# Optimization experiments

Hardware: AMD Instinct MI355X
Metric: run time of the kernel (lower is better)

Reference implementation:

```python
import jax, jax.numpy as jnp
import numpy as np

YOLO_INTERVAL = 20.0
N_BOXES = 4_000_000
N_ANCHORS = 5
N_CELLS = 12  # image_size // yolo_interval


def setup_inputs() -> dict:
    key = jax.random.key(0)
    k1, k2, k3 = jax.random.split(key, 3)
    cell_nos = jax.random.randint(k1, (N_BOXES, 2), 0, N_CELLS, dtype=jnp.int32)
    output = jax.random.uniform(k2, (N_BOXES, N_ANCHORS, 5), dtype=jnp.float32)
    target = jax.random.uniform(k3, (N_BOXES, 5), dtype=jnp.float32)
    return {"cell_nos": cell_nos, "output": output, "target": target}


def _bbox_to_corners(cell_nos, dx, dy, h, w):
    # cell_nos: [N,2] int; dx,dy,h,w: [N,K] float. Returns [N,K,4] (x1,y1,x2,y2).
    yi = YOLO_INTERVAL
    h = h * yi
    w = w * yi
    cell_i_center = cell_nos[:, 0:1].astype(dx.dtype) * yi + yi / 2  # [N,1]
    cell_j_center = cell_nos[:, 1:2].astype(dx.dtype) * yi + yi / 2
    x_center = cell_i_center + dx * yi  # broadcast [N,K]
    y_center = cell_j_center + dy * yi
    x1 = y_center - w / 2
    y1 = x_center - h / 2
    x2 = y_center + w / 2
    y2 = x_center + h / 2
    return jnp.stack([x1, y1, x2, y2], axis=-1)


def reference(cell_nos, output, target):
    # Predicted boxes: [N, A, 4]
    dxp, dyp, hp, wp = (output[:, :, i] for i in range(1, 5))
    bbox_pred = _bbox_to_corners(cell_nos, dxp, dyp, hp, wp)
    # Ground-truth boxes: [N, 4]
    dxg, dyg, hg, wg = (target[:, i:i + 1] for i in range(1, 5))
    bbox_gt = _bbox_to_corners(cell_nos, dxg, dyg, hg, wg)[:, 0, :]
    # Elementwise IoU (the original computed full NxN box_iou and took the diagonal)
    area_p = (bbox_pred[..., 2] - bbox_pred[..., 0]) * (bbox_pred[..., 3] - bbox_pred[..., 1])  # [N,A]
    area_g = (bbox_gt[:, 2] - bbox_gt[:, 0]) * (bbox_gt[:, 3] - bbox_gt[:, 1])  # [N]
    lt = jnp.maximum(bbox_pred[..., :2], bbox_gt[:, None, :2])  # [N,A,2]
    rb = jnp.minimum(bbox_pred[..., 2:], bbox_gt[:, None, 2:])
    wh = jnp.clip(rb - lt, 0.0)
    inter = wh[..., 0] * wh[..., 1]  # [N,A]
    union = area_p + area_g[:, None] - inter
    return inter / union
```

## Files before the change

### kernel.cpp

```cpp
#include <hip/hip_runtime.h>


#define YI 20.0f
#define BOXES_PER_BLK 256

__global__ __launch_bounds__(256) void iou_kernel(
    const int*   __restrict__ cell,
    const float* __restrict__ outp,
    const float* __restrict__ tgt,
    float*       __restrict__ dst,
    int nboxes)
{
    __shared__ float s_out[BOXES_PER_BLK * 25];
    __shared__ float s_tgt[BOXES_PER_BLK * 5];
    __shared__ int   s_cell[BOXES_PER_BLK * 2];

    const int t = threadIdx.x;
    const long long base = (long long)blockIdx.x * BOXES_PER_BLK;
    const bool full_block = (base + BOXES_PER_BLK) <= (long long)nboxes;

    if (full_block) {
        {
            const float4* g = reinterpret_cast<const float4*>(outp + base * 25);
            float4* s = reinterpret_cast<float4*>(s_out);
            #pragma unroll
            for (int i = t; i < (BOXES_PER_BLK * 25) / 4; i += BOXES_PER_BLK) s[i] = g[i];
        }
        {
            const float4* g = reinterpret_cast<const float4*>(tgt + base * 5);
            float4* s = reinterpret_cast<float4*>(s_tgt);
            #pragma unroll
            for (int i = t; i < (BOXES_PER_BLK * 5) / 4; i += BOXES_PER_BLK) s[i] = g[i];
        }
        {
            const int4* g = reinterpret_cast<const int4*>(cell + base * 2);
            int4* s = reinterpret_cast<int4*>(s_cell);
            if (t < (BOXES_PER_BLK * 2) / 4) s[t] = g[t];
        }
        __syncthreads();

        const float* my_out = &s_out[t * 25];
        const float* my_tgt = &s_tgt[t * 5];
        const float ci = (float)s_cell[t * 2 + 0];
        const float cj = (float)s_cell[t * 2 + 1];
        const float cic = ci * YI + 0.5f * YI;
        const float cjc = cj * YI + 0.5f * YI;

        const float dxg = my_tgt[1], dyg = my_tgt[2];
        const float hg = my_tgt[3] * YI, wg = my_tgt[4] * YI;
        const float xcg = cic + dxg * YI, ycg = cjc + dyg * YI;
        const float x1g = ycg - 0.5f * wg, y1g = xcg - 0.5f * hg;
        const float x2g = ycg + 0.5f * wg, y2g = xcg + 0.5f * hg;
        const float area_g = (x2g - x1g) * (y2g - y1g);

        float res[5];
        #pragma unroll
        for (int a = 0; a < 5; ++a) {
            const float dx = my_out[5 * a + 1], dy = my_out[5 * a + 2];
            const float h = my_out[5 * a + 3] * YI, w = my_out[5 * a + 4] * YI;
            const float xc = cic + dx * YI, yc = cjc + dy * YI;
            const float x1 = yc - 0.5f * w, y1 = xc - 0.5f * h;
            const float x2 = yc + 0.5f * w, y2 = xc + 0.5f * h;
            const float area_p = (x2 - x1) * (y2 - y1);
            const float ltx = fmaxf(x1, x1g), lty = fmaxf(y1, y1g);
            const float rbx = fminf(x2, x2g), rby = fminf(y2, y2g);
            const float wx = fmaxf(rbx - ltx, 0.0f), wy = fmaxf(rby - lty, 0.0f);
            const float inter = wx * wy;
            const float uni = area_p + area_g - inter;
            res[a] = inter / uni;
        }

        #pragma unroll
        for (int a = 0; a < 5; ++a) s_tgt[t * 5 + a] = res[a];
        __syncthreads();

        {
            float4* g = reinterpret_cast<float4*>(dst + base * 5);
            const float4* s = reinterpret_cast<const float4*>(s_tgt);
            #pragma unroll
            for (int i = t; i < (BOXES_PER_BLK * 5) / 4; i += BOXES_PER_BLK) g[i] = s[i];
        }
    } else {
        const long long n = base + t;
        if (n < (long long)nboxes) {
            const float ci = (float)cell[n * 2 + 0];
            const float cj = (float)cell[n * 2 + 1];
            const float cic = ci * YI + 0.5f * YI;
            const float cjc = cj * YI + 0.5f * YI;
            const float dxg = tgt[n * 5 + 1], dyg = tgt[n * 5 + 2];
            const float hg = tgt[n * 5 + 3] * YI, wg = tgt[n * 5 + 4] * YI;
            const float xcg = cic + dxg * YI, ycg = cjc + dyg * YI;
            const float x1g = ycg - 0.5f * wg, y1g = xcg - 0.5f * hg;
            const float x2g = ycg + 0.5f * wg, y2g = xcg + 0.5f * hg;
            const float area_g = (x2g - x1g) * (y2g - y1g);
            for (int a = 0; a < 5; ++a) {
                const float dx = outp[n * 25 + 5 * a + 1], dy = outp[n * 25 + 5 * a + 2];
                const float h = outp[n * 25 + 5 * a + 3] * YI, w = outp[n * 25 + 5 * a + 4] * YI;
                const float xc = cic + dx * YI, yc = cjc + dy * YI;
                const float x1 = yc - 0.5f * w, y1 = xc - 0.5f * h;
                const float x2 = yc + 0.5f * w, y2 = xc + 0.5f * h;
                const float area_p = (x2 - x1) * (y2 - y1);
                const float ltx = fmaxf(x1, x1g), lty = fmaxf(y1, y1g);
                const float rbx = fminf(x2, x2g), rby = fminf(y2, y2g);
                const float wx = fmaxf(rbx - ltx, 0.0f), wy = fmaxf(rby - lty, 0.0f);
                const float inter = wx * wy;
                const float uni = area_p + area_g - inter;
                dst[n * 5 + a] = inter / uni;
            }
        }
    }
}

extern "C" void kernel_launch(void* const* d_in, const int* in_sizes, int n_in,
                              void* d_out, int out_size, void* d_ws, size_t ws_size,
                              hipStream_t stream) {
    const int*   cell = (const int*)d_in[0];
    const float* outp = (const float*)d_in[1];
    const float* tgt  = (const float*)d_in[2];
    float*       dst  = (float*)d_out;

    const int nboxes = in_sizes[0] / 2;
    const int grid = (nboxes + BOXES_PER_BLK - 1) / BOXES_PER_BLK;
    iou_kernel<<<grid, BOXES_PER_BLK, 0, stream>>>(cell, outp, tgt, dst, nboxes);
}
```

Before: 599.4 us.

## Map one thread per box-anchor pair and drop shared-memory staging

Replaces the block-per-256-boxes kernel, which staged outputs, targets and cells through LDS with float4 loads, with an elementwise kernel where each thread computes one (box, anchor) IoU straight from global memory. This removes the LDS traffic, the barriers and the large shared allocation that limits occupancy, and it launches five times as many threads. In exchange, global loads become strided scalar accesses, and each target and cell row is read redundantly by five threads, relying on cache for coalescing.

Result: no change. 592.1 us (-1.2%).

```diff
diff --git a/kernel.cpp b/kernel.cpp
--- a/kernel.cpp
+++ b/kernel.cpp
@@ -2,113 +2,56 @@
 
 
 #define YI 20.0f
-#define BOXES_PER_BLK 256
 
-__global__ __launch_bounds__(256) void iou_kernel(
+__global__ __launch_bounds__(256) void iou_elem(
     const int*   __restrict__ cell,
     const float* __restrict__ outp,
     const float* __restrict__ tgt,
     float*       __restrict__ dst,
-    int nboxes)
+    int total)
 {
-    __shared__ float s_out[BOXES_PER_BLK * 25];
-    __shared__ float s_tgt[BOXES_PER_BLK * 5];
-    __shared__ int   s_cell[BOXES_PER_BLK * 2];
+    const int tid = blockIdx.x * 256 + threadIdx.x;
+    if (tid >= total) return;
 
-    const int t = threadIdx.x;
-    const long long base = (long long)blockIdx.x * BOXES_PER_BLK;
-    const bool full_block = (base + BOXES_PER_BLK) <= (long long)nboxes;
+    const unsigned n = (unsigned)tid / 5u;
+    const unsigned a = (unsigned)tid - 5u * n;
 
-    if (full_block) {
-        {
-            const float4* g = reinterpret_cast<const float4*>(outp + base * 25);
-            float4* s = reinterpret_cast<float4*>(s_out);
-            #pragma unroll
-            for (int i = t; i < (BOXES_PER_BLK * 25) / 4; i += BOXES_PER_BLK) s[i] = g[i];
-        }
-        {
-            const float4* g = reinterpret_cast<const float4*>(tgt + base * 5);
-            float4* s = reinterpret_cast<float4*>(s_tgt);
-            #pragma unroll
-            for (int i = t; i < (BOXES_PER_BLK * 5) / 4; i += BOXES_PER_BLK) s[i] = g[i];
-        }
-        {
-            const int4* g = reinterpret_cast<const int4*>(cell + base * 2);
-            int4* s = reinterpret_cast<int4*>(s_cell);
-            if (t < (BOXES_PER_BLK * 2) / 4) s[t] = g[t];
-        }
-        __syncthreads();
+    const float* op = outp + (size_t)n * 25 + (size_t)a * 5;
+    const float dx = op[1];
+    const float dy = op[2];
+    const float hr = op[3];
+    const float wr = op[4];
 
-        const float* my_out = &s_out[t * 25];
-        const float* my_tgt = &s_tgt[t * 5];
-        const float ci = (float)s_cell[t * 2 + 0];
-        const float cj = (float)s_cell[t * 2 + 1];
-        const float cic = ci * YI + 0.5f * YI;
-        const float cjc = cj * YI + 0.5f * YI;
+    const float* tp = tgt + (size_t)n * 5;
+    const float dxg = tp[1];
+    const float dyg = tp[2];
+    const float hgr = tp[3];
+    const float wgr = tp[4];
 
-        const float dxg = my_tgt[1], dyg = my_tgt[2];
-        const float hg = my_tgt[3] * YI, wg = my_tgt[4] * YI;
-        const float xcg = cic + dxg * YI, ycg = cjc + dyg * YI;
-        const float x1g = ycg - 0.5f * wg, y1g = xcg - 0.5f * hg;
-        const float x2g = ycg + 0.5f * wg, y2g = xcg + 0.5f * hg;
-        const float area_g = (x2g - x1g) * (y2g - y1g);
+    const int2 c = reinterpret_cast<const int2*>(cell)[n];
 
-        float res[5];
-        #pragma unroll
-        for (int a = 0; a < 5; ++a) {
-            const float dx = my_out[5 * a + 1], dy = my_out[5 * a + 2];
-            const float h = my_out[5 * a + 3] * YI, w = my_out[5 * a + 4] * YI;
-            const float xc = cic + dx * YI, yc = cjc + dy * YI;
-            const float x1 = yc - 0.5f * w, y1 = xc - 0.5f * h;
-            const float x2 = yc + 0.5f * w, y2 = xc + 0.5f * h;
-            const float area_p = (x2 - x1) * (y2 - y1);
-            const float ltx = fmaxf(x1, x1g), lty = fmaxf(y1, y1g);
-            const float rbx = fminf(x2, x2g), rby = fminf(y2, y2g);
-            const float wx = fmaxf(rbx - ltx, 0.0f), wy = fmaxf(rby - lty, 0.0f);
-            const float inter = wx * wy;
-            const float uni = area_p + area_g - inter;
-            res[a] = inter / uni;
-        }
+    const float cic = (float)c.x * YI + 0.5f * YI;
+    const float cjc = (float)c.y * YI + 0.5f * YI;
 
-        #pragma unroll
-        for (int a = 0; a < 5; ++a) s_tgt[t * 5 + a] = res[a];
-        __syncthreads();
+    const float hg = hgr * YI, wg = wgr * YI;
+    const float xcg = cic + dxg * YI, ycg = cjc + dyg * YI;
+    const float x1g = ycg - 0.5f * wg, y1g = xcg - 0.5f * hg;
+    const float x2g = ycg + 0.5f * wg, y2g = xcg + 0.5f * hg;
+    const float area_g = (x2g - x1g) * (y2g - y1g);
 
-        {
-            float4* g = reinterpret_cast<float4*>(dst + base * 5);
-            const float4* s = reinterpret_cast<const float4*>(s_tgt);
-            #pragma unroll
-            for (int i = t; i < (BOXES_PER_BLK * 5) / 4; i += BOXES_PER_BLK) g[i] = s[i];
-        }
-    } else {
-        const long long n = base + t;
-        if (n < (long long)nboxes) {
-            const float ci = (float)cell[n * 2 + 0];
-            const float cj = (float)cell[n * 2 + 1];
-            const float cic = ci * YI + 0.5f * YI;
-            const float cjc = cj * YI + 0.5f * YI;
-            const float dxg = tgt[n * 5 + 1], dyg = tgt[n * 5 + 2];
-            const float hg = tgt[n * 5 + 3] * YI, wg = tgt[n * 5 + 4] * YI;
-            const float xcg = cic + dxg * YI, ycg = cjc + dyg * YI;
-            const float x1g = ycg - 0.5f * wg, y1g = xcg - 0.5f * hg;
-            const float x2g = ycg + 0.5f * wg, y2g = xcg + 0.5f * hg;
-            const float area_g = (x2g - x1g) * (y2g - y1g);
-            for (int a = 0; a < 5; ++a) {
-                const float dx = outp[n * 25 + 5 * a + 1], dy = outp[n * 25 + 5 * a + 2];
-                const float h = outp[n * 25 + 5 * a + 3] * YI, w = outp[n * 25 + 5 * a + 4] * YI;
-                const float xc = cic + dx * YI, yc = cjc + dy * YI;
-                const float x1 = yc - 0.5f * w, y1 = xc - 0.5f * h;
-                const float x2 = yc + 0.5f * w, y2 = xc + 0.5f * h;
-                const float area_p = (x2 - x1) * (y2 - y1);
-                const float ltx = fmaxf(x1, x1g), lty = fmaxf(y1, y1g);
-                const float rbx = fminf(x2, x2g), rby = fminf(y2, y2g);
-                const float wx = fmaxf(rbx - ltx, 0.0f), wy = fmaxf(rby - lty, 0.0f);
-                const float inter = wx * wy;
-                const float uni = area_p + area_g - inter;
-                dst[n * 5 + a] = inter / uni;
-            }
-        }
-    }
+    const float h = hr * YI, w = wr * YI;
+    const float xc = cic + dx * YI, yc = cjc + dy * YI;
+    const float x1 = yc - 0.5f * w, y1 = xc - 0.5f * h;
+    const float x2 = yc + 0.5f * w, y2 = xc + 0.5f * h;
+    const float area_p = (x2 - x1) * (y2 - y1);
+
+    const float ltx = fmaxf(x1, x1g), lty = fmaxf(y1, y1g);
+    const float rbx = fminf(x2, x2g), rby = fminf(y2, y2g);
+    const float wx = fmaxf(rbx - ltx, 0.0f), wy = fmaxf(rby - lty, 0.0f);
+    const float inter = wx * wy;
+    const float uni = area_p + area_g - inter;
+
+    dst[tid] = inter / uni;
 }
 
 extern "C" void kernel_launch(void* const* d_in, const int* in_sizes, int n_in,
@@ -119,7 +62,7 @@
     const float* tgt  = (const float*)d_in[2];
     float*       dst  = (float*)d_out;
 
-    const int nboxes = in_sizes[0] / 2;
-    const int grid = (nboxes + BOXES_PER_BLK - 1) / BOXES_PER_BLK;
-    iou_kernel<<<grid, BOXES_PER_BLK, 0, stream>>>(cell, outp, tgt, dst, nboxes);
+    const int total = out_size;
+    const int grid = (total + 255) / 256;
+    iou_elem<<<grid, 256, 0, stream>>>(cell, outp, tgt, dst, total);
 }
```
